# Kernel tuning notes

Measured on AMD Instinct MI355X. Metric: run time of the kernel, lower is better.

## Reference

```python
import jax, jax.numpy as jnp
import numpy as np

N = 262144
H = 256
POS_L, DIR_L = 10, 4


def _encode(x, L):
    # classic NeRF sinusoidal encoding with identity: [N,3] -> [N, 3 + 6*L]
    f = 2.0 ** jnp.arange(L, dtype=x.dtype)          # [L]
    xf = x[:, :, None] * f                            # [N,3,L]
    n = x.shape[0]
    return jnp.concatenate([x, jnp.sin(xf).reshape(n, -1), jnp.cos(xf).reshape(n, -1)], axis=1)


def setup_inputs() -> dict:
    key = jax.random.key(0)
    ks = iter(jax.random.split(key, 32))
    inp = {
        "pos": jax.random.normal(next(ks), (N, 3), jnp.float32),
        "dir": jax.random.normal(next(ks), (N, 3), jnp.float32),
        "pixel_width": jax.random.uniform(next(ks), (N, 1), dtype=jnp.float32),
        "t_start": jax.random.uniform(next(ks), (N, 1), dtype=jnp.float32),
        "t_end": jax.random.uniform(next(ks), (N, 1), dtype=jnp.float32),
    }
    pe_dim = 3 + 6 * POS_L   # 63
    de_dim = 3 + 6 * DIR_L   # 27
    dims = {
        "w00": (pe_dim, H), "w01": (H, H), "w02": (H, H), "w03": (H, H),
        "w10": (H + pe_dim, H), "w11": (H, H), "w12": (H, H), "w13": (H, H),
        "cw0": (H + de_dim, H // 2), "cw1": (H // 2, 4),
    }
    for name, (i, o) in dims.items():
        inp[name] = jax.random.normal(next(ks), (i, o), jnp.float32) * (1.0 / np.sqrt(i))
        inp[name.replace("w", "b", 1)] = jnp.zeros((o,), jnp.float32)
    return inp


def _nerf(pos, dir, w00, b00, w01, b01, w02, b02, w03, b03,
          w10, b10, w11, b11, w12, b12, w13, b13, cw0, cb0, cw1, cb1):
    pe = _encode(pos, POS_L)   # [N,63]
    de = _encode(dir, DIR_L)   # [N,27]
    r = jax.nn.relu
    # segment 0 (4 linears, ReLU between all, plus inter-segment ReLU)
    z = r(pe @ w00 + b00)
    z = r(z @ w01 + b01)
    z = r(z @ w02 + b02)
    z = r(z @ w03 + b03)
    # segment 1: positional encoding re-concatenated (skip connection)
    z = jnp.concatenate([z, pe], axis=1)              # [N,319]
    z = r(z @ w10 + b10)
    z = r(z @ w11 + b11)
    z = r(z @ w12 + b12)
    z = z @ w13 + b13                                 # no activation after last segment
    # color head: direction encoding concatenated (delayed_direction=True)
    h = r(jnp.concatenate([z, de], axis=1) @ cw0 + cb0)   # [N,128]
    out = h @ cw1 + cb1                                    # [N,4] (rgb + density, delayed_density=True)
    d = out[:, -1]
    density = jnp.where(d > 8.0, d, jax.nn.softplus(d))    # Softplus(threshold=8)
    rgb = jax.nn.sigmoid(out[:, :3])
    return density, rgb


def reference(pos, dir, pixel_width, t_start, t_end,
              w00, b00, w01, b01, w02, b02, w03, b03,
              w10, b10, w11, b11, w12, b12, w13, b13,
              cw0, cb0, cw1, cb1):
    # pixel_width / t_start / t_end are consumed only by mip-style encoders; the
    # classic sinusoidal encoder used here ignores them (kept for signature parity).
    return _nerf(pos, dir, w00, b00, w01, b01, w02, b02, w03, b03,
                 w10, b10, w11, b11, w12, b12, w13, b13, cw0, cb0, cw1, cb1)
```

## Files before the change

kernel.cpp:

```cpp
#include <hip/hip_runtime.h>
#include <hip/hip_bf16.h>
#include <math.h>

typedef unsigned short u16;
typedef unsigned int   u32;
typedef __bf16 bf16x8 __attribute__((ext_vector_type(8)));
typedef float  f32x4  __attribute__((ext_vector_type(4)));

#define NRAYS 262144
#define NBLK  (NRAYS / 64)

enum : size_t { PO0=0, PO1=16384, PO2=81920, PO3=147456, PO4=212992,
                PO5=294912, PO6=360448, PO7=425984, PO8=491520, PO9=528384 };
#define TOTAL_PACK_ELEMS 530432

__device__ __forceinline__ u16 f2bf(float x) {
  u32 u = __float_as_uint(x);
  u32 r = (u + 0x7FFFu + ((u >> 16) & 1u)) >> 16;
  return (u16)r;
}

struct PackArgs {
  const float* src[10];
  int K[10];
  int N[10];
  int l2mt[10];
  int cstart[11];
};

__global__ __launch_bounds__(256) void pack_w(PackArgs a, u16* __restrict__ dst)
{
  int e = blockIdx.x * 256 + threadIdx.x;
  if (e >= TOTAL_PACK_ELEMS) return;
  int chunk = e >> 9;
  int li = 0;
  #pragma unroll
  for (int t = 1; t < 10; ++t) li += (chunk >= a.cstart[t]) ? 1 : 0;
  int lc = chunk - a.cstart[li];
  int ks = lc >> a.l2mt[li];
  int mt = lc - (ks << a.l2mt[li]);
  int lane = (e >> 3) & 63, j = e & 7;
  int k = ks * 32 + ((lane >> 4) << 3) + j;
  int n = mt * 16 + (lane & 15);
  float v = 0.f;
  if (k < a.K[li] && n < a.N[li]) v = a.src[li][(size_t)k * a.N[li] + n];
  dst[e] = f2bf(v);
}

template<int M>
__device__ __forceinline__ void zacc(f32x4 a[M][4]) {
  #pragma unroll
  for (int i = 0; i < M; ++i)
    #pragma unroll
    for (int j = 0; j < 4; ++j) a[i][j] = (f32x4){0.f, 0.f, 0.f, 0.f};
}

template<int MT_W, int NSTEPS>
__device__ __forceinline__ void gseg(f32x4 acc[MT_W][4],
    const u16* __restrict__ act, int astride,
    const u16* __restrict__ wl, int mt_total, int mt0, int ksbase, int lane)
{
  const int lhi = (lane >> 4) << 3, llo = lane & 15;
  #pragma unroll
  for (int ks = 0; ks < NSTEPS; ++ks) {
    const u16* ap = act + (size_t)llo * astride + ks * 32 + lhi;
    bf16x8 b[4];
    #pragma unroll
    for (int nt = 0; nt < 4; ++nt)
      b[nt] = *(const bf16x8*)(ap + (size_t)nt * 16 * astride);
    const u16* wp = wl + ((size_t)(ksbase + ks) * mt_total + mt0) * 512 + lane * 8;
    bf16x8 a[MT_W];
    #pragma unroll
    for (int mt = 0; mt < MT_W; ++mt)
      a[mt] = *(const bf16x8*)(wp + (size_t)mt * 512);
    #pragma unroll
    for (int mt = 0; mt < MT_W; ++mt)
      #pragma unroll
      for (int nt = 0; nt < 4; ++nt)
        acc[mt][nt] = __builtin_amdgcn_mfma_f32_16x16x32_bf16(a[mt], b[nt], acc[mt][nt], 0, 0, 0);
  }
}

template<int MT_W, bool RELU>
__device__ __forceinline__ void zstore(f32x4 acc[MT_W][4],
    const float* __restrict__ bias, int ch0, u16* dst, int dstride, int lane)
{
  const int llo = lane & 15, cq = (lane >> 4) << 2;
  #pragma unroll
  for (int mt = 0; mt < MT_W; ++mt) {
    int ch = ch0 + mt * 16 + cq;
    float4 bv = *(const float4*)(bias + ch);
    #pragma unroll
    for (int nt = 0; nt < 4; ++nt) {
      f32x4 v = acc[mt][nt];
      float x0 = v.x + bv.x, x1 = v.y + bv.y, x2 = v.z + bv.z, x3 = v.w + bv.w;
      if (RELU) { x0 = fmaxf(x0, 0.f); x1 = fmaxf(x1, 0.f);
                  x2 = fmaxf(x2, 0.f); x3 = fmaxf(x3, 0.f); }
      uint2 pk;
      pk.x = (u32)f2bf(x0) | ((u32)f2bf(x1) << 16);
      pk.y = (u32)f2bf(x2) | ((u32)f2bf(x3) << 16);
      *(uint2*)(dst + (size_t)(nt * 16 + llo) * dstride + ch) = pk;
    }
  }
}

__global__ __launch_bounds__(256, 3) void nerf_fused(
    const float* __restrict__ pos,  const float* __restrict__ dirv,
    const float* __restrict__ b00,  const float* __restrict__ b01,
    const float* __restrict__ b02,  const float* __restrict__ b03,
    const float* __restrict__ b10,  const float* __restrict__ b11,
    const float* __restrict__ b12,  const float* __restrict__ b13,
    const float* __restrict__ cb0,  const float* __restrict__ cb1,
    const u16* __restrict__ W, float* __restrict__ out)
{
  __shared__ __align__(16) u16 zb[64 * 264];
  __shared__ __align__(16) u16 peb[64 * 72];
  __shared__ __align__(16) u16 deb[64 * 40];
  __shared__ float xyz[64 * 6];

  const int tid = threadIdx.x;
  const int rb  = blockIdx.x * 64;
  const int lane = tid & 63, wid = tid >> 6;

  if (tid < 192) {
    int r = tid / 3, c = tid - r * 3;
    xyz[r * 6 + c]     = pos[(size_t)(rb + r) * 3 + c];
    xyz[r * 6 + 3 + c] = dirv[(size_t)(rb + r) * 3 + c];
  }
  __syncthreads();

  for (int i = tid; i < 64 * 30; i += 256) {
    int r = i / 30, t = i - r * 30;
    int j = t / 10, l = t - j * 10;
    float x = xyz[r * 6 + j] * (float)(1 << l);
    float s, c; sincosf(x, &s, &c);
    peb[r * 72 + 3 + t]  = f2bf(s);
    peb[r * 72 + 33 + t] = f2bf(c);
  }
  for (int i = tid; i < 64 * 4; i += 256) {
    int r = i >> 2, c = i & 3;
    peb[r * 72 + (c < 3 ? c : 63)] = (c < 3) ? f2bf(xyz[r * 6 + c]) : (u16)0;
  }
  for (int i = tid; i < 64 * 12; i += 256) {
    int r = i / 12, t = i - r * 12;
    int j = t >> 2, l = t & 3;
    float x = xyz[r * 6 + 3 + j] * (float)(1 << l);
    float s, c; sincosf(x, &s, &c);
    deb[r * 40 + 3 + t]  = f2bf(s);
    deb[r * 40 + 15 + t] = f2bf(c);
  }
  for (int i = tid; i < 64 * 8; i += 256) {
    int r = i >> 3, c = i & 7;
    deb[r * 40 + (c < 3 ? c : 24 + c)] = (c < 3) ? f2bf(xyz[r * 6 + 3 + c]) : (u16)0;
  }
  __syncthreads();

  f32x4 acc[4][4];

  zacc<4>(acc);
  gseg<4, 2>(acc, peb, 72, W + PO0, 16, wid * 4, 0, lane);
  __syncthreads();
  zstore<4, true>(acc, b00, wid * 64, zb, 264, lane);
  __syncthreads();
  zacc<4>(acc);
  gseg<4, 8>(acc, zb, 264, W + PO1, 16, wid * 4, 0, lane);
  __syncthreads();
  zstore<4, true>(acc, b01, wid * 64, zb, 264, lane);
  __syncthreads();
  zacc<4>(acc);
  gseg<4, 8>(acc, zb, 264, W + PO2, 16, wid * 4, 0, lane);
  __syncthreads();
  zstore<4, true>(acc, b02, wid * 64, zb, 264, lane);
  __syncthreads();
  zacc<4>(acc);
  gseg<4, 8>(acc, zb, 264, W + PO3, 16, wid * 4, 0, lane);
  __syncthreads();
  zstore<4, true>(acc, b03, wid * 64, zb, 264, lane);
  __syncthreads();
  zacc<4>(acc);
  gseg<4, 8>(acc, zb, 264, W + PO4, 16, wid * 4, 0, lane);
  gseg<4, 2>(acc, peb, 72, W + PO4, 16, wid * 4, 8, lane);
  __syncthreads();
  zstore<4, true>(acc, b10, wid * 64, zb, 264, lane);
  __syncthreads();
  zacc<4>(acc);
  gseg<4, 8>(acc, zb, 264, W + PO5, 16, wid * 4, 0, lane);
  __syncthreads();
  zstore<4, true>(acc, b11, wid * 64, zb, 264, lane);
  __syncthreads();
  zacc<4>(acc);
  gseg<4, 8>(acc, zb, 264, W + PO6, 16, wid * 4, 0, lane);
  __syncthreads();
  zstore<4, true>(acc, b12, wid * 64, zb, 264, lane);
  __syncthreads();
  zacc<4>(acc);
  gseg<4, 8>(acc, zb, 264, W + PO7, 16, wid * 4, 0, lane);
  __syncthreads();
  zstore<4, false>(acc, b13, wid * 64, zb, 264, lane);
  __syncthreads();
  {
    f32x4 acc2[2][4];
    zacc<2>(acc2);
    gseg<2, 8>(acc2, zb, 264, W + PO8, 8, wid * 2, 0, lane);
    gseg<2, 1>(acc2, deb, 40, W + PO8, 8, wid * 2, 8, lane);
    __syncthreads();
    zstore<2, true>(acc2, cb0, wid * 32, zb, 264, lane);
    __syncthreads();
  }
  {
    const u16* W9 = W + PO9;
    const int lhi = (lane >> 4) << 3, llo = lane & 15;
    f32x4 c9 = (f32x4){0.f, 0.f, 0.f, 0.f};
    #pragma unroll
    for (int ks = 0; ks < 4; ++ks) {
      bf16x8 b = *(const bf16x8*)(zb + (size_t)(wid * 16 + llo) * 264 + ks * 32 + lhi);
      bf16x8 a = *(const bf16x8*)(W9 + (size_t)ks * 512 + lane * 8);
      c9 = __builtin_amdgcn_mfma_f32_16x16x32_bf16(a, b, c9, 0, 0, 0);
    }
    if ((lane >> 4) == 0) {
      int ray = rb + wid * 16 + llo;
      float o0 = c9.x + cb1[0];
      float o1 = c9.y + cb1[1];
      float o2 = c9.z + cb1[2];
      float dv = c9.w + cb1[3];
      out[ray] = (dv > 8.f) ? dv : log1pf(expf(dv));
      float* rgb = out + NRAYS + (size_t)ray * 3;
      rgb[0] = 1.f / (1.f + expf(-o0));
      rgb[1] = 1.f / (1.f + expf(-o1));
      rgb[2] = 1.f / (1.f + expf(-o2));
    }
  }
}

extern "C" void kernel_launch(void* const* d_in, const int* in_sizes, int n_in,
                              void* d_out, int out_size, void* d_ws, size_t ws_size,
                              hipStream_t stream)
{
  (void)in_sizes; (void)n_in; (void)out_size; (void)ws_size;
  const float* pos  = (const float*)d_in[0];
  const float* dirv = (const float*)d_in[1];
  PackArgs pa;
  const int widx[10] = {5, 7, 9, 11, 13, 15, 17, 19, 21, 23};
  const int K[10]    = {63, 256, 256, 256, 319, 256, 256, 256, 283, 128};
  const int Nn[10]   = {256, 256, 256, 256, 256, 256, 256, 256, 128, 4};
  const int L2MT[10] = {4, 4, 4, 4, 4, 4, 4, 4, 3, 0};
  const int CS[11]   = {0, 32, 160, 288, 416, 576, 704, 832, 960, 1032, 1036};
  for (int i = 0; i < 10; ++i) {
    pa.src[i] = (const float*)d_in[widx[i]];
    pa.K[i] = K[i]; pa.N[i] = Nn[i]; pa.l2mt[i] = L2MT[i];
  }
  for (int i = 0; i < 11; ++i) pa.cstart[i] = CS[i];

  u16* wp = (u16*)d_ws;
  hipLaunchKernelGGL(pack_w, dim3(TOTAL_PACK_ELEMS / 256), dim3(256), 0, stream, pa, wp);

  hipLaunchKernelGGL(nerf_fused, dim3(NBLK), dim3(256), 0, stream,
      pos, dirv,
      (const float*)d_in[6],  (const float*)d_in[8],
      (const float*)d_in[10], (const float*)d_in[12],
      (const float*)d_in[14], (const float*)d_in[16],
      (const float*)d_in[18], (const float*)d_in[20],
      (const float*)d_in[22], (const float*)d_in[24],
      wp, (float*)d_out);
}
```

Baseline: 369.8 us.

## Merge LDS buffers into one XOR-swizzled tile and raise occupancy

Replaces the three padded LDS buffers (activations, position encoding, direction encoding) with a single 64x320 bf16 tile that uses an XOR swizzle on 8-element column groups. The encodings live in the tail columns, and the direction encoding is computed late, after segment 1's first layer. This cuts LDS footprint so launch bounds can rise to 4 blocks per SM, and the swizzle aims to remove bank conflicts. It also moves the bias into accumulator initialisation, switches to round-half-up bf16 conversion, and uses fast __sinf/__cosf/__expf. The fast intrinsics and the changed rounding add precision risk, especially __sinf on position inputs scaled up to 512.

```diff
diff --git a/kernel.cpp b/kernel.cpp
--- a/kernel.cpp
+++ b/kernel.cpp
@@ -10,22 +10,17 @@
 #define NRAYS 262144
 #define NBLK  (NRAYS / 64)
 
-enum : size_t { PO0=0, PO1=16384, PO2=81920, PO3=147456, PO4=212992,
-                PO5=294912, PO6=360448, PO7=425984, PO8=491520, PO9=528384 };
+enum : int { PO0=0, PO1=16384, PO2=81920, PO3=147456, PO4=212992,
+             PO5=294912, PO6=360448, PO7=425984, PO8=491520, PO9=528384 };
 #define TOTAL_PACK_ELEMS 530432
 
 __device__ __forceinline__ u16 f2bf(float x) {
-  u32 u = __float_as_uint(x);
-  u32 r = (u + 0x7FFFu + ((u >> 16) & 1u)) >> 16;
-  return (u16)r;
+  return (u16)((__float_as_uint(x) + 0x8000u) >> 16);
 }
 
 struct PackArgs {
   const float* src[10];
-  int K[10];
-  int N[10];
-  int l2mt[10];
-  int cstart[11];
+  int K[10]; int N[10]; int l2mt[10]; int cstart[11];
 };
 
 __global__ __launch_bounds__(256) void pack_w(PackArgs a, u16* __restrict__ dst)
@@ -44,35 +39,47 @@
   int n = mt * 16 + (lane & 15);
   float v = 0.f;
   if (k < a.K[li] && n < a.N[li]) v = a.src[li][(size_t)k * a.N[li] + n];
-  dst[e] = f2bf(v);
-}
-
-template<int M>
-__device__ __forceinline__ void zacc(f32x4 a[M][4]) {
-  #pragma unroll
-  for (int i = 0; i < M; ++i)
-    #pragma unroll
-    for (int j = 0; j < 4; ++j) a[i][j] = (f32x4){0.f, 0.f, 0.f, 0.f};
-}
-
-template<int MT_W, int NSTEPS>
+  u32 u = __float_as_uint(v);
+  dst[e] = (u16)((u + 0x7FFFu + ((u >> 16) & 1u)) >> 16);
+}
+
+__device__ __forceinline__ void wr_enc(u16* zb, int r, int c, u16 v) {
+  zb[r * 320 + ((((c >> 3) ^ (r & 7))) << 3) + (c & 7)] = v;
+}
+
+template<int MT_W>
+__device__ __forceinline__ void binit(f32x4 acc[MT_W][4],
+    const float* __restrict__ bias, int chbase, int lane)
+{
+  const int q = lane >> 4;
+  #pragma unroll
+  for (int mt = 0; mt < MT_W; ++mt) {
+    float4 bv = *(const float4*)(bias + chbase + mt * 16 + q * 4);
+    #pragma unroll
+    for (int nt = 0; nt < 4; ++nt)
+      acc[mt][nt] = (f32x4){bv.x, bv.y, bv.z, bv.w};
+  }
+}
+
+template<int MT_W, int NSTEPS, int MT_TOTAL>
 __device__ __forceinline__ void gseg(f32x4 acc[MT_W][4],
-    const u16* __restrict__ act, int astride,
-    const u16* __restrict__ wl, int mt_total, int mt0, int ksbase, int lane)
-{
-  const int lhi = (lane >> 4) << 3, llo = lane & 15;
+    const u16* __restrict__ zb, int cbase8,
+    const u16* __restrict__ wl, int mt0, int ksbase, int lane)
+{
+  const int q = lane >> 4, llo = lane & 15;
   #pragma unroll
   for (int ks = 0; ks < NSTEPS; ++ks) {
-    const u16* ap = act + (size_t)llo * astride + ks * 32 + lhi;
+    int c8s = ((cbase8 + ks * 4 + q) ^ (llo & 7));
+    const u16* bp = zb + llo * 320 + c8s * 8;
     bf16x8 b[4];
     #pragma unroll
     for (int nt = 0; nt < 4; ++nt)
-      b[nt] = *(const bf16x8*)(ap + (size_t)nt * 16 * astride);
-    const u16* wp = wl + ((size_t)(ksbase + ks) * mt_total + mt0) * 512 + lane * 8;
+      b[nt] = *(const bf16x8*)(bp + nt * 16 * 320);
+    int widx = ((ksbase + ks) * MT_TOTAL + mt0) * 512 + lane * 8;
     bf16x8 a[MT_W];
     #pragma unroll
     for (int mt = 0; mt < MT_W; ++mt)
-      a[mt] = *(const bf16x8*)(wp + (size_t)mt * 512);
+      a[mt] = *(const bf16x8*)(wl + widx + mt * 512);
     #pragma unroll
     for (int mt = 0; mt < MT_W; ++mt)
       #pragma unroll
@@ -83,28 +90,32 @@
 
 template<int MT_W, bool RELU>
 __device__ __forceinline__ void zstore(f32x4 acc[MT_W][4],
-    const float* __restrict__ bias, int ch0, u16* dst, int dstride, int lane)
-{
-  const int llo = lane & 15, cq = (lane >> 4) << 2;
+    int chbase, u16* zb, int lane)
+{
+  const int llo = lane & 15, q = lane >> 4;
   #pragma unroll
   for (int mt = 0; mt < MT_W; ++mt) {
-    int ch = ch0 + mt * 16 + cq;
-    float4 bv = *(const float4*)(bias + ch);
+    int ch = chbase + mt * 16 + q * 4;
+    int off0 = (((ch >> 3) ^ (llo & 7)) << 3) + (ch & 7);
     #pragma unroll
     for (int nt = 0; nt < 4; ++nt) {
       f32x4 v = acc[mt][nt];
-      float x0 = v.x + bv.x, x1 = v.y + bv.y, x2 = v.z + bv.z, x3 = v.w + bv.w;
+      float x0 = v.x, x1 = v.y, x2 = v.z, x3 = v.w;
       if (RELU) { x0 = fmaxf(x0, 0.f); x1 = fmaxf(x1, 0.f);
                   x2 = fmaxf(x2, 0.f); x3 = fmaxf(x3, 0.f); }
+      u32 a0 = __float_as_uint(x0) + 0x8000u;
+      u32 a1 = __float_as_uint(x1) + 0x8000u;
+      u32 a2 = __float_as_uint(x2) + 0x8000u;
+      u32 a3 = __float_as_uint(x3) + 0x8000u;
       uint2 pk;
-      pk.x = (u32)f2bf(x0) | ((u32)f2bf(x1) << 16);
-      pk.y = (u32)f2bf(x2) | ((u32)f2bf(x3) << 16);
-      *(uint2*)(dst + (size_t)(nt * 16 + llo) * dstride + ch) = pk;
-    }
-  }
-}
-
-__global__ __launch_bounds__(256, 3) void nerf_fused(
+      pk.x = (a1 & 0xFFFF0000u) | (a0 >> 16);
+      pk.y = (a3 & 0xFFFF0000u) | (a2 >> 16);
+      *(uint2*)(zb + (nt * 16 + llo) * 320 + off0) = pk;
+    }
+  }
+}
+
+__global__ __launch_bounds__(256, 4) void nerf_fused(
     const float* __restrict__ pos,  const float* __restrict__ dirv,
     const float* __restrict__ b00,  const float* __restrict__ b01,
     const float* __restrict__ b02,  const float* __restrict__ b03,
@@ -113,10 +124,8 @@
     const float* __restrict__ cb0,  const float* __restrict__ cb1,
     const u16* __restrict__ W, float* __restrict__ out)
 {
-  __shared__ __align__(16) u16 zb[64 * 264];
-  __shared__ __align__(16) u16 peb[64 * 72];
-  __shared__ __align__(16) u16 deb[64 * 40];
-  __shared__ float xyz[64 * 6];
+  __shared__ __align__(16) u16 zb[64 * 320];
+  float* xyzf = (float*)zb;
 
   const int tid = threadIdx.x;
   const int rb  = blockIdx.x * 64;
@@ -124,110 +133,121 @@
 
   if (tid < 192) {
     int r = tid / 3, c = tid - r * 3;
-    xyz[r * 6 + c]     = pos[(size_t)(rb + r) * 3 + c];
-    xyz[r * 6 + 3 + c] = dirv[(size_t)(rb + r) * 3 + c];
-  }
-  __syncthreads();
-
-  for (int i = tid; i < 64 * 30; i += 256) {
-    int r = i / 30, t = i - r * 30;
-    int j = t / 10, l = t - j * 10;
-    float x = xyz[r * 6 + j] * (float)(1 << l);
-    float s, c; sincosf(x, &s, &c);
-    peb[r * 72 + 3 + t]  = f2bf(s);
-    peb[r * 72 + 33 + t] = f2bf(c);
-  }
-  for (int i = tid; i < 64 * 4; i += 256) {
-    int r = i >> 2, c = i & 3;
-    peb[r * 72 + (c < 3 ? c : 63)] = (c < 3) ? f2bf(xyz[r * 6 + c]) : (u16)0;
-  }
-  for (int i = tid; i < 64 * 12; i += 256) {
-    int r = i / 12, t = i - r * 12;
-    int j = t >> 2, l = t & 3;
-    float x = xyz[r * 6 + 3 + j] * (float)(1 << l);
-    float s, c; sincosf(x, &s, &c);
-    deb[r * 40 + 3 + t]  = f2bf(s);
-    deb[r * 40 + 15 + t] = f2bf(c);
-  }
-  for (int i = tid; i < 64 * 8; i += 256) {
-    int r = i >> 3, c = i & 7;
-    deb[r * 40 + (c < 3 ? c : 24 + c)] = (c < 3) ? f2bf(xyz[r * 6 + 3 + c]) : (u16)0;
+    xyzf[r * 160 + c] = pos[(size_t)(rb + r) * 3 + c];
+  }
+  __syncthreads();
+
+  #pragma unroll
+  for (int i = tid; i < 64 * 32; i += 256) {
+    int r = i >> 5, t = i & 31;
+    if (t < 30) {
+      int j = t / 10, l = t - j * 10;
+      float x = xyzf[r * 160 + j] * (float)(1 << l);
+      wr_enc(zb, r, 256 + 3 + t,  f2bf(__sinf(x)));
+      wr_enc(zb, r, 256 + 33 + t, f2bf(__cosf(x)));
+    }
+  }
+  {
+    int r = tid >> 2, c = tid & 3;
+    u16 v = 0; int col = 63;
+    if (c < 3) { col = c; v = f2bf(xyzf[r * 160 + c]); }
+    wr_enc(zb, r, 256 + col, v);
   }
   __syncthreads();
 
   f32x4 acc[4][4];
 
-  zacc<4>(acc);
-  gseg<4, 2>(acc, peb, 72, W + PO0, 16, wid * 4, 0, lane);
-  __syncthreads();
-  zstore<4, true>(acc, b00, wid * 64, zb, 264, lane);
-  __syncthreads();
-  zacc<4>(acc);
-  gseg<4, 8>(acc, zb, 264, W + PO1, 16, wid * 4, 0, lane);
-  __syncthreads();
-  zstore<4, true>(acc, b01, wid * 64, zb, 264, lane);
-  __syncthreads();
-  zacc<4>(acc);
-  gseg<4, 8>(acc, zb, 264, W + PO2, 16, wid * 4, 0, lane);
-  __syncthreads();
-  zstore<4, true>(acc, b02, wid * 64, zb, 264, lane);
-  __syncthreads();
-  zacc<4>(acc);
-  gseg<4, 8>(acc, zb, 264, W + PO3, 16, wid * 4, 0, lane);
-  __syncthreads();
-  zstore<4, true>(acc, b03, wid * 64, zb, 264, lane);
-  __syncthreads();
-  zacc<4>(acc);
-  gseg<4, 8>(acc, zb, 264, W + PO4, 16, wid * 4, 0, lane);
-  gseg<4, 2>(acc, peb, 72, W + PO4, 16, wid * 4, 8, lane);
-  __syncthreads();
-  zstore<4, true>(acc, b10, wid * 64, zb, 264, lane);
-  __syncthreads();
-  zacc<4>(acc);
-  gseg<4, 8>(acc, zb, 264, W + PO5, 16, wid * 4, 0, lane);
-  __syncthreads();
-  zstore<4, true>(acc, b11, wid * 64, zb, 264, lane);
-  __syncthreads();
-  zacc<4>(acc);
-  gseg<4, 8>(acc, zb, 264, W + PO6, 16, wid * 4, 0, lane);
-  __syncthreads();
-  zstore<4, true>(acc, b12, wid * 64, zb, 264, lane);
-  __syncthreads();
-  zacc<4>(acc);
-  gseg<4, 8>(acc, zb, 264, W + PO7, 16, wid * 4, 0, lane);
-  __syncthreads();
-  zstore<4, false>(acc, b13, wid * 64, zb, 264, lane);
+  binit<4>(acc, b00, wid * 64, lane);
+  gseg<4, 2, 16>(acc, zb, 32, W + PO0, wid * 4, 0, lane);
+  __syncthreads();
+  zstore<4, true>(acc, wid * 64, zb, lane);
+  __syncthreads();
+  binit<4>(acc, b01, wid * 64, lane);
+  gseg<4, 8, 16>(acc, zb, 0, W + PO1, wid * 4, 0, lane);
+  __syncthreads();
+  zstore<4, true>(acc, wid * 64, zb, lane);
+  __syncthreads();
+  binit<4>(acc, b02, wid * 64, lane);
+  gseg<4, 8, 16>(acc, zb, 0, W + PO2, wid * 4, 0, lane);
+  __syncthreads();
+  zstore<4, true>(acc, wid * 64, zb, lane);
+  __syncthreads();
+  binit<4>(acc, b03, wid * 64, lane);
+  gseg<4, 8, 16>(acc, zb, 0, W + PO3, wid * 4, 0, lane);
+  __syncthreads();
+  zstore<4, true>(acc, wid * 64, zb, lane);
+  __syncthreads();
+  binit<4>(acc, b10, wid * 64, lane);
+  gseg<4, 8, 16>(acc, zb, 0,  W + PO4, wid * 4, 0, lane);
+  gseg<4, 2, 16>(acc, zb, 32, W + PO4, wid * 4, 8, lane);
+  __syncthreads();
+  zstore<4, true>(acc, wid * 64, zb, lane);
+  #pragma unroll
+  for (int i = tid; i < 64 * 16; i += 256) {
+    int r = i >> 4, t = i & 15;
+    if (t < 12) {
+      int j = t >> 2, l = t & 3;
+      float x = dirv[(size_t)(rb + r) * 3 + j] * (float)(1 << l);
+      wr_enc(zb, r, 288 + 3 + t,  f2bf(__sinf(x)));
+      wr_enc(zb, r, 288 + 15 + t, f2bf(__cosf(x)));
+    } else {
+      wr_enc(zb, r, 288 + 15 + t, 0);
+    }
+  }
+  {
+    int r = tid >> 2, c = tid & 3;
+    u16 v = 0; int col = 31;
+    if (c < 3) { col = c; v = f2bf(dirv[(size_t)(rb + r) * 3 + c]); }
+    wr_enc(zb, r, 288 + col, v);
+  }
+  __syncthreads();
+  binit<4>(acc, b11, wid * 64, lane);
+  gseg<4, 8, 16>(acc, zb, 0, W + PO5, wid * 4, 0, lane);
+  __syncthreads();
+  zstore<4, true>(acc, wid * 64, zb, lane);
+  __syncthreads();
+  binit<4>(acc, b12, wid * 64, lane);
+  gseg<4, 8, 16>(acc, zb, 0, W + PO6, wid * 4, 0, lane);
+  __syncthreads();
+  zstore<4, true>(acc, wid * 64, zb, lane);
+  __syncthreads();
+  binit<4>(acc, b13, wid * 64, lane);
+  gseg<4, 8, 16>(acc, zb, 0, W + PO7, wid * 4, 0, lane);
+  __syncthreads();
+  zstore<4, false>(acc, wid * 64, zb, lane);
   __syncthreads();
   {
     f32x4 acc2[2][4];
-    zacc<2>(acc2);
-    gseg<2, 8>(acc2, zb, 264, W + PO8, 8, wid * 2, 0, lane);
-    gseg<2, 1>(acc2, deb, 40, W + PO8, 8, wid * 2, 8, lane);
+    binit<2>(acc2, cb0, wid * 32, lane);
+    gseg<2, 8, 8>(acc2, zb, 0,  W + PO8, wid * 2, 0, lane);
+    gseg<2, 1, 8>(acc2, zb, 36, W + PO8, wid * 2, 8, lane);
     __syncthreads();
-    zstore<2, true>(acc2, cb0, wid * 32, zb, 264, lane);
+    zstore<2, true>(acc2, wid * 32, zb, lane);
     __syncthreads();
   }
   {
     const u16* W9 = W + PO9;
-    const int lhi = (lane >> 4) << 3, llo = lane & 15;
+    const int q = lane >> 4, llo = lane & 15;
+    const int r = wid * 16 + llo;
     f32x4 c9 = (f32x4){0.f, 0.f, 0.f, 0.f};
     #pragma unroll
     for (int ks = 0; ks < 4; ++ks) {
-      bf16x8 b = *(const bf16x8*)(zb + (size_t)(wid * 16 + llo) * 264 + ks * 32 + lhi);
-      bf16x8 a = *(const bf16x8*)(W9 + (size_t)ks * 512 + lane * 8);
+      int c8s = ((ks * 4 + q) ^ (llo & 7));
+      bf16x8 b = *(const bf16x8*)(zb + r * 320 + c8s * 8);
+      bf16x8 a = *(const bf16x8*)(W9 + ks * 512 + lane * 8);
       c9 = __builtin_amdgcn_mfma_f32_16x16x32_bf16(a, b, c9, 0, 0, 0);
     }
-    if ((lane >> 4) == 0) {
-      int ray = rb + wid * 16 + llo;
+    if (q == 0) {
+      int ray = rb + r;
       float o0 = c9.x + cb1[0];
       float o1 = c9.y + cb1[1];
       float o2 = c9.z + cb1[2];
       float dv = c9.w + cb1[3];
-      out[ray] = (dv > 8.f) ? dv : log1pf(expf(dv));
+      out[ray] = (dv > 8.f) ? dv : log1pf(__expf(dv));
       float* rgb = out + NRAYS + (size_t)ray * 3;
-      rgb[0] = 1.f / (1.f + expf(-o0));
-      rgb[1] = 1.f / (1.f + expf(-o1));
-      rgb[2] = 1.f / (1.f + expf(-o2));
+      rgb[0] = 1.f / (1.f + __expf(-o0));
+      rgb[1] = 1.f / (1.f + __expf(-o1));
+      rgb[2] = 1.f / (1.f + __expf(-o2));
     }
   }
 }
```

Result: slower. 421.5 us (+14.0%).
